# Kernel tuning notes

Measured on AMD Instinct MI355X. Metric: run time of the kernel, lower is better.

Reference implementation:

```python
import jax, jax.numpy as jnp
import numpy as np

WINDOW_SIZE = 5
SIGMA = 1.5


def gaussian_kernel_3d(size, sigma):
    # Faithful replication of the torch code (including its permute quirk):
    # kernel[i,j,k] = exp(-((k-off)^2 + (k-off)^2 + (i-off)^2) / (2*sigma^2))
    c = jnp.arange(size, dtype=jnp.float32) - size // 2
    ci = c[:, None, None]  # axis 0 term (from permute(2,0,1))
    ck = c[None, None, :]  # axis 2 term (coords and permute(1,0,2) coincide)
    g = jnp.exp(-(ck ** 2 + ck ** 2 + ci ** 2) / (2.0 * sigma ** 2))
    g = jnp.broadcast_to(g, (size, size, size))
    return g / g.sum()


def _conv3d(x, w, pad):
    # x: [N,C,D,H,W], w: [O,I,kd,kh,kw]
    return jax.lax.conv_general_dilated(
        x, w, window_strides=(1, 1, 1),
        padding=[(pad, pad)] * 3,
        dimension_numbers=('NCDHW', 'OIDHW', 'NCDHW'))


def setup_inputs() -> dict:
    key = jax.random.key(0)
    k1, k2 = jax.random.split(key)
    img1 = jax.random.uniform(k1, (4, 2, 128, 128, 128), dtype=jnp.float32)
    img2 = jax.random.uniform(k2, (4, 1, 128, 128, 128), dtype=jnp.float32)
    window = gaussian_kernel_3d(WINDOW_SIZE, SIGMA)[None, None]  # [1,1,5,5,5]
    return {"img1": img1, "img2": img2, "window": window}


def reference(img1, img2, window):
    ws = window.shape[-1]
    pad = ws // 2
    x1 = img1[:, 1:2]  # select channel 1, keep dim -> [B,1,D,H,W]
    x2 = img2
    mu1 = _conv3d(x1, window, pad)
    mu2 = _conv3d(x2, window, pad)
    mu1_sq = mu1 * mu1
    mu2_sq = mu2 * mu2
    mu1_mu2 = mu1 * mu2
    sigma1_sq = _conv3d(x1 * x1, window, pad) - mu1_sq
    sigma2_sq = _conv3d(x2 * x2, window, pad) - mu2_sq
    sigma12 = _conv3d(x1 * x2, window, pad) - mu1_mu2
    C1 = 0.01 ** 2
    C2 = 0.03 ** 2
    ssim_map = ((2.0 * mu1_mu2 + C1) * (2.0 * sigma12 + C2)) / (
        (mu1_sq + mu2_sq + C1) * (sigma1_sq + sigma2_sq + C2))
    return 1.0 - jnp.mean(ssim_map)
```

## Files before the change

### kernel.cpp

```cpp
#include <hip/hip_runtime.h>


#define NDIM 128
#define TH 4
#define WR (TH + 4)
#define DSUB 16
#define NHT (NDIM / TH)
#define NDT (NDIM / DSUB)
#define NB 4
#define NBLK (NHT * NDT * NB)

__global__ void factorize_window(const float* __restrict__ w, float* __restrict__ ws) {
    if (threadIdx.x == 0) {
        float w000 = w[0];
        #pragma unroll
        for (int i = 0; i < 5; ++i) ws[i]      = w[i * 25];
        #pragma unroll
        for (int j = 0; j < 5; ++j) ws[5 + j]  = w[j * 5] / w000;
        #pragma unroll
        for (int k = 0; k < 5; ++k) ws[10 + k] = w[k] / w000;
    }
}

__launch_bounds__(256, 4)
__global__ void ssim_main(const float* __restrict__ img1,
                          const float* __restrict__ img2,
                          const float* __restrict__ wfac,
                          float* __restrict__ partials) {
    const int bid = blockIdx.x;
    const int th = bid % NHT;
    const int td = (bid / NHT) % NDT;
    const int b  = bid / (NHT * NDT);

    const int h0 = th * TH, d0 = td * DSUB;
    const float* __restrict__ x1 = img1 + (size_t)(b * 2 + 1) * NDIM * NDIM * NDIM;
    const float* __restrict__ x2 = img2 + (size_t)b * NDIM * NDIM * NDIM;

    float uW[5], vW[5], tW[5];
    #pragma unroll
    for (int i = 0; i < 5; ++i) { uW[i] = wfac[i]; vW[i] = wfac[5 + i]; tW[i] = wfac[10 + i]; }

    __shared__ float sWc[5][WR][NDIM];
    __shared__ float sRed[4];

    const int tid  = threadIdx.x;
    const int wrow = tid >> 5;
    const int wcg  = tid & 31;
    const int c0   = wcg * 4;
    const int ghw  = h0 + wrow - 2;
    const int orow = tid >> 6;
    const int oc   = (tid & 63) * 2;

    float2 ring[5][5];
    float2 accS = make_float2(0.f, 0.f);

#define PHASE(I, P) do {                                                       \
    const int i_ = (I);                                                        \
    const int d_ = d0 - 2 + i_;                                                \
    float4 A0 = make_float4(0,0,0,0), A1 = A0, A2 = A0;                        \
    float4 B0 = A0, B1 = A0, B2 = A0;                                          \
    if (((unsigned)d_ < NDIM) && ((unsigned)ghw < NDIM)) {                     \
        const float* __restrict__ r1_ = x1 + ((size_t)d_ * NDIM + ghw) * NDIM; \
        const float* __restrict__ r2_ = x2 + ((size_t)d_ * NDIM + ghw) * NDIM; \
        if (wcg > 0)  { A0 = *(const float4*)(r1_ + c0 - 4);                   \
                        B0 = *(const float4*)(r2_ + c0 - 4); }                 \
        A1 = *(const float4*)(r1_ + c0);                                       \
        B1 = *(const float4*)(r2_ + c0);                                       \
        if (wcg < 31) { A2 = *(const float4*)(r1_ + c0 + 4);                   \
                        B2 = *(const float4*)(r2_ + c0 + 4); }                 \
    }                                                                          \
    float ra[12] = {A0.x,A0.y,A0.z,A0.w, A1.x,A1.y,A1.z,A1.w,                  \
                    A2.x,A2.y,A2.z,A2.w};                                      \
    float rb[12] = {B0.x,B0.y,B0.z,B0.w, B1.x,B1.y,B1.z,B1.w,                  \
                    B2.x,B2.y,B2.z,B2.w};                                      \
    float m1v[4], m2v[4], q11v[4], q22v[4], q12v[4];                           \
    _Pragma("unroll")                                                          \
    for (int k_ = 0; k_ < 4; ++k_) {                                           \
        float m1_=0.f, m2_=0.f, q11_=0.f, q22_=0.f, q12_=0.f;                  \
        _Pragma("unroll")                                                      \
        for (int c_ = 0; c_ < 5; ++c_) {                                       \
            const float a_ = ra[k_ + c_ + 2], b_ = rb[k_ + c_ + 2];            \
            const float ta_ = tW[c_] * a_, tb_ = tW[c_] * b_;                  \
            m1_ += ta_; m2_ += tb_;                                            \
            q11_ += ta_ * a_; q22_ += tb_ * b_; q12_ += ta_ * b_;              \
        }                                                                      \
        m1v[k_]=m1_; m2v[k_]=m2_; q11v[k_]=q11_; q22v[k_]=q22_; q12v[k_]=q12_; \
    }                                                                          \
    __syncthreads();                   \
    *(float4*)&sWc[0][wrow][c0] = make_float4(m1v[0],m1v[1],m1v[2],m1v[3]);    \
    *(float4*)&sWc[1][wrow][c0] = make_float4(m2v[0],m2v[1],m2v[2],m2v[3]);    \
    *(float4*)&sWc[2][wrow][c0] = make_float4(q11v[0],q11v[1],q11v[2],q11v[3]);\
    *(float4*)&sWc[3][wrow][c0] = make_float4(q22v[0],q22v[1],q22v[2],q22v[3]);\
    *(float4*)&sWc[4][wrow][c0] = make_float4(q12v[0],q12v[1],q12v[2],q12v[3]);\
    __syncthreads();                                       \
    _Pragma("unroll")                                                          \
    for (int f_ = 0; f_ < 5; ++f_) {                                           \
        float2 F_ = make_float2(0.f, 0.f);                                     \
        _Pragma("unroll")                                                      \
        for (int r_ = 0; r_ < 5; ++r_) {                                       \
            const float2 wv_ = *(const float2*)&sWc[f_][orow + r_][oc];        \
            F_.x += vW[r_] * wv_.x;                                            \
            F_.y += vW[r_] * wv_.y;                                            \
        }                                                                      \
        ring[(P)][f_] = F_;                                                    \
    }                                                                          \
    if (i_ >= 4) {                                                             \
        float2 F0 = make_float2(0,0), F1 = F0, F2 = F0, F3 = F0, F4 = F0;      \
        _Pragma("unroll")                                                      \
        for (int j_ = 0; j_ < 5; ++j_) {                                       \
            const int s_ = ((P) + 1 + j_) % 5;                                 \
            const float uw_ = uW[j_];                                          \
            F0.x += uw_*ring[s_][0].x; F0.y += uw_*ring[s_][0].y;              \
            F1.x += uw_*ring[s_][1].x; F1.y += uw_*ring[s_][1].y;              \
            F2.x += uw_*ring[s_][2].x; F2.y += uw_*ring[s_][2].y;              \
            F3.x += uw_*ring[s_][3].x; F3.y += uw_*ring[s_][3].y;              \
            F4.x += uw_*ring[s_][4].x; F4.y += uw_*ring[s_][4].y;              \
        }                                                                      \
        {                                                                      \
            const float mu1 = F0.x, mu2 = F1.x;                                \
            const float m11 = mu1*mu1, m22 = mu2*mu2, m12 = mu1*mu2;           \
            const float num = (2.f*m12 + 1e-4f) * (2.f*(F4.x - m12) + 9e-4f);  \
            const float den = (m11 + m22 + 1e-4f) *                            \
                              ((F2.x - m11) + (F3.x - m22) + 9e-4f);           \
            accS.x += __fdividef(num, den);                                    \
        }                                                                      \
        {                                                                      \
            const float mu1 = F0.y, mu2 = F1.y;                                \
            const float m11 = mu1*mu1, m22 = mu2*mu2, m12 = mu1*mu2;           \
            const float num = (2.f*m12 + 1e-4f) * (2.f*(F4.y - m12) + 9e-4f);  \
            const float den = (m11 + m22 + 1e-4f) *                            \
                              ((F2.y - m11) + (F3.y - m22) + 9e-4f);           \
            accS.y += __fdividef(num, den);                                    \
        }                                                                      \
    }                                                                          \
} while (0)

    for (int io = 0; io < 4; ++io) {
        const int ib = io * 5;
        PHASE(ib + 0, 0);
        PHASE(ib + 1, 1);
        PHASE(ib + 2, 2);
        PHASE(ib + 3, 3);
        PHASE(ib + 4, 4);
    }
#undef PHASE

    float acc = accS.x + accS.y;
    #pragma unroll
    for (int off = 32; off > 0; off >>= 1)
        acc += __shfl_down(acc, off, 64);
    __syncthreads();
    if ((tid & 63) == 0) sRed[tid >> 6] = acc;
    __syncthreads();
    if (tid == 0) partials[bid] = sRed[0] + sRed[1] + sRed[2] + sRed[3];
}

__global__ void finalize_kernel(const float* __restrict__ partials, float* __restrict__ out) {
    const int tid = threadIdx.x;
    double s = 0.0;
    for (int i = tid; i < NBLK; i += 256) s += (double)partials[i];
    #pragma unroll
    for (int off = 32; off > 0; off >>= 1)
        s += __shfl_down(s, off, 64);
    __shared__ double sm[4];
    if ((tid & 63) == 0) sm[tid >> 6] = s;
    __syncthreads();
    if (tid == 0)
        out[0] = 1.0f - (float)((sm[0] + sm[1] + sm[2] + sm[3]) / (double)(4LL * 128 * 128 * 128));
}

extern "C" void kernel_launch(void* const* d_in, const int* in_sizes, int n_in,
                              void* d_out, int out_size, void* d_ws, size_t ws_size,
                              hipStream_t stream) {
    const float* img1 = (const float*)d_in[0];
    const float* img2 = (const float*)d_in[1];
    const float* win  = (const float*)d_in[2];
    float* out = (float*)d_out;
    float* ws  = (float*)d_ws;
    float* wfac     = ws;
    float* partials = ws + 16;

    hipLaunchKernelGGL(factorize_window, dim3(1), dim3(64), 0, stream, win, wfac);
    hipLaunchKernelGGL(ssim_main, dim3(NBLK), dim3(256), 0, stream, img1, img2, wfac, partials);
    hipLaunchKernelGGL(finalize_kernel, dim3(1), dim3(256), 0, stream, partials, out);
}
```

Baseline: 162.6 us.

## Double-buffer shared tile, prefetch next depth slice, fuse final reduction via atomics

Each depth slice's global loads are now issued into registers one phase ahead, so they overlap with the current slice's shared-memory stores and vertical pass. The shared staging buffer is double-buffered, which removes one of the two barriers per phase. The separate finalize kernel is replaced by a double atomicAdd plus a last-block counter, which saves a launch. In exchange, shared memory per block doubles, which may lower occupancy, and the prefetch registers add register pressure.

```diff
diff --git a/kernel.cpp b/kernel.cpp
--- a/kernel.cpp
+++ b/kernel.cpp
@@ -10,23 +10,25 @@
 #define NB 4
 #define NBLK (NHT * NDT * NB)
 
-__global__ void factorize_window(const float* __restrict__ w, float* __restrict__ ws) {
+__global__ void setup_kernel(const float* __restrict__ w, float* __restrict__ ws) {
     if (threadIdx.x == 0) {
-        float w000 = w[0];
+        const float w000 = w[0];
         #pragma unroll
         for (int i = 0; i < 5; ++i) ws[i]      = w[i * 25];
         #pragma unroll
         for (int j = 0; j < 5; ++j) ws[5 + j]  = w[j * 5] / w000;
         #pragma unroll
         for (int k = 0; k < 5; ++k) ws[10 + k] = w[k] / w000;
+        *(double*)(ws + 16)       = 0.0;
+        *(unsigned int*)(ws + 18) = 0u;
     }
 }
 
 __launch_bounds__(256, 4)
 __global__ void ssim_main(const float* __restrict__ img1,
                           const float* __restrict__ img2,
-                          const float* __restrict__ wfac,
-                          float* __restrict__ partials) {
+                          float* __restrict__ wsp,
+                          float* __restrict__ out) {
     const int bid = blockIdx.x;
     const int th = bid % NHT;
     const int td = (bid / NHT) % NDT;
@@ -38,10 +40,9 @@
 
     float uW[5], vW[5], tW[5];
     #pragma unroll
-    for (int i = 0; i < 5; ++i) { uW[i] = wfac[i]; vW[i] = wfac[5 + i]; tW[i] = wfac[10 + i]; }
+    for (int i = 0; i < 5; ++i) { uW[i] = wsp[i]; vW[i] = wsp[5 + i]; tW[i] = wsp[10 + i]; }
 
-    __shared__ float sWc[5][WR][NDIM];
-    __shared__ float sRed[4];
+    __shared__ float sWc[2][5][WR][NDIM];
 
     const int tid  = threadIdx.x;
     const int wrow = tid >> 5;
@@ -53,26 +54,33 @@
 
     float2 ring[5][5];
     float2 accS = make_float2(0.f, 0.f);
+    float4 ld[6];
 
-#define PHASE(I, P) do {                                                       \
+#define LOADP(IN) do {                                                         \
+    const int ip_ = (IN);                                                      \
+    const int dp_ = d0 - 2 + ip_;                                              \
+    const float4 z_ = make_float4(0.f, 0.f, 0.f, 0.f);                         \
+    ld[0]=z_; ld[1]=z_; ld[2]=z_; ld[3]=z_; ld[4]=z_; ld[5]=z_;                \
+    if ((ip_ < DSUB + 4) && ((unsigned)dp_ < NDIM) && ((unsigned)ghw < NDIM)) {\
+        const float* __restrict__ r1_ = x1 + ((size_t)dp_ * NDIM + ghw) * NDIM;\
+        const float* __restrict__ r2_ = x2 + ((size_t)dp_ * NDIM + ghw) * NDIM;\
+        if (wcg > 0)  { ld[0] = *(const float4*)(r1_ + c0 - 4);                \
+                        ld[3] = *(const float4*)(r2_ + c0 - 4); }              \
+        ld[1] = *(const float4*)(r1_ + c0);                                    \
+        ld[4] = *(const float4*)(r2_ + c0);                                    \
+        if (wcg < 31) { ld[2] = *(const float4*)(r1_ + c0 + 4);                \
+                        ld[5] = *(const float4*)(r2_ + c0 + 4); }              \
+    }                                                                          \
+} while (0)
+
+#define PHASE(I, P, B) do {                                                    \
     const int i_ = (I);                                                        \
-    const int d_ = d0 - 2 + i_;                                                \
-    float4 A0 = make_float4(0,0,0,0), A1 = A0, A2 = A0;                        \
-    float4 B0 = A0, B1 = A0, B2 = A0;                                          \
-    if (((unsigned)d_ < NDIM) && ((unsigned)ghw < NDIM)) {                     \
-        const float* __restrict__ r1_ = x1 + ((size_t)d_ * NDIM + ghw) * NDIM; \
-        const float* __restrict__ r2_ = x2 + ((size_t)d_ * NDIM + ghw) * NDIM; \
-        if (wcg > 0)  { A0 = *(const float4*)(r1_ + c0 - 4);                   \
-                        B0 = *(const float4*)(r2_ + c0 - 4); }                 \
-        A1 = *(const float4*)(r1_ + c0);                                       \
-        B1 = *(const float4*)(r2_ + c0);                                       \
-        if (wcg < 31) { A2 = *(const float4*)(r1_ + c0 + 4);                   \
-                        B2 = *(const float4*)(r2_ + c0 + 4); }                 \
-    }                                                                          \
-    float ra[12] = {A0.x,A0.y,A0.z,A0.w, A1.x,A1.y,A1.z,A1.w,                  \
-                    A2.x,A2.y,A2.z,A2.w};                                      \
-    float rb[12] = {B0.x,B0.y,B0.z,B0.w, B1.x,B1.y,B1.z,B1.w,                  \
-                    B2.x,B2.y,B2.z,B2.w};                                      \
+    float ra[12] = {ld[0].x,ld[0].y,ld[0].z,ld[0].w,                           \
+                    ld[1].x,ld[1].y,ld[1].z,ld[1].w,                           \
+                    ld[2].x,ld[2].y,ld[2].z,ld[2].w};                          \
+    float rb[12] = {ld[3].x,ld[3].y,ld[3].z,ld[3].w,                           \
+                    ld[4].x,ld[4].y,ld[4].z,ld[4].w,                           \
+                    ld[5].x,ld[5].y,ld[5].z,ld[5].w};                          \
     float m1v[4], m2v[4], q11v[4], q22v[4], q12v[4];                           \
     _Pragma("unroll")                                                          \
     for (int k_ = 0; k_ < 4; ++k_) {                                           \
@@ -86,23 +94,23 @@
         }                                                                      \
         m1v[k_]=m1_; m2v[k_]=m2_; q11v[k_]=q11_; q22v[k_]=q22_; q12v[k_]=q12_; \
     }                                                                          \
-    __syncthreads();                   \
-    *(float4*)&sWc[0][wrow][c0] = make_float4(m1v[0],m1v[1],m1v[2],m1v[3]);    \
-    *(float4*)&sWc[1][wrow][c0] = make_float4(m2v[0],m2v[1],m2v[2],m2v[3]);    \
-    *(float4*)&sWc[2][wrow][c0] = make_float4(q11v[0],q11v[1],q11v[2],q11v[3]);\
-    *(float4*)&sWc[3][wrow][c0] = make_float4(q22v[0],q22v[1],q22v[2],q22v[3]);\
-    *(float4*)&sWc[4][wrow][c0] = make_float4(q12v[0],q12v[1],q12v[2],q12v[3]);\
-    __syncthreads();                                       \
+    LOADP(i_ + 1);    \
+    *(float4*)&sWc[B][0][wrow][c0] = make_float4(m1v[0],m1v[1],m1v[2],m1v[3]); \
+    *(float4*)&sWc[B][1][wrow][c0] = make_float4(m2v[0],m2v[1],m2v[2],m2v[3]); \
+    *(float4*)&sWc[B][2][wrow][c0] = make_float4(q11v[0],q11v[1],q11v[2],q11v[3]);\
+    *(float4*)&sWc[B][3][wrow][c0] = make_float4(q22v[0],q22v[1],q22v[2],q22v[3]);\
+    *(float4*)&sWc[B][4][wrow][c0] = make_float4(q12v[0],q12v[1],q12v[2],q12v[3]);\
+    __syncthreads();            \
     _Pragma("unroll")                                                          \
     for (int f_ = 0; f_ < 5; ++f_) {                                           \
         float2 F_ = make_float2(0.f, 0.f);                                     \
         _Pragma("unroll")                                                      \
         for (int r_ = 0; r_ < 5; ++r_) {                                       \
-            const float2 wv_ = *(const float2*)&sWc[f_][orow + r_][oc];        \
+            const float2 wv_ = *(const float2*)&sWc[B][f_][orow + r_][oc];     \
             F_.x += vW[r_] * wv_.x;                                            \
             F_.y += vW[r_] * wv_.y;                                            \
         }                                                                      \
-        ring[(P)][f_] = F_;                                                    \
+        ring[P][f_] = F_;                                                      \
     }                                                                          \
     if (i_ >= 4) {                                                             \
         float2 F0 = make_float2(0,0), F1 = F0, F2 = F0, F3 = F0, F4 = F0;      \
@@ -135,38 +143,43 @@
     }                                                                          \
 } while (0)
 
-    for (int io = 0; io < 4; ++io) {
-        const int ib = io * 5;
-        PHASE(ib + 0, 0);
-        PHASE(ib + 1, 1);
-        PHASE(ib + 2, 2);
-        PHASE(ib + 3, 3);
-        PHASE(ib + 4, 4);
+    LOADP(0);
+    for (int io = 0; io < 2; ++io) {
+        const int ib = io * 10;
+        PHASE(ib + 0, 0, 0);
+        PHASE(ib + 1, 1, 1);
+        PHASE(ib + 2, 2, 0);
+        PHASE(ib + 3, 3, 1);
+        PHASE(ib + 4, 4, 0);
+        PHASE(ib + 5, 0, 1);
+        PHASE(ib + 6, 1, 0);
+        PHASE(ib + 7, 2, 1);
+        PHASE(ib + 8, 3, 0);
+        PHASE(ib + 9, 4, 1);
     }
 #undef PHASE
+#undef LOADP
 
     float acc = accS.x + accS.y;
     #pragma unroll
     for (int off = 32; off > 0; off >>= 1)
         acc += __shfl_down(acc, off, 64);
     __syncthreads();
-    if ((tid & 63) == 0) sRed[tid >> 6] = acc;
+    float* sred = &sWc[0][0][0][0];
+    if ((tid & 63) == 0) sred[tid >> 6] = acc;
     __syncthreads();
-    if (tid == 0) partials[bid] = sRed[0] + sRed[1] + sRed[2] + sRed[3];
-}
-
-__global__ void finalize_kernel(const float* __restrict__ partials, float* __restrict__ out) {
-    const int tid = threadIdx.x;
-    double s = 0.0;
-    for (int i = tid; i < NBLK; i += 256) s += (double)partials[i];
-    #pragma unroll
-    for (int off = 32; off > 0; off >>= 1)
-        s += __shfl_down(s, off, 64);
-    __shared__ double sm[4];
-    if ((tid & 63) == 0) sm[tid >> 6] = s;
-    __syncthreads();
-    if (tid == 0)
-        out[0] = 1.0f - (float)((sm[0] + sm[1] + sm[2] + sm[3]) / (double)(4LL * 128 * 128 * 128));
+    if (tid == 0) {
+        const float bsum = sred[0] + sred[1] + sred[2] + sred[3];
+        double* accg      = (double*)(wsp + 16);
+        unsigned int* cnt = (unsigned int*)(wsp + 18);
+        atomicAdd(accg, (double)bsum);
+        __threadfence();
+        const unsigned int prev = atomicAdd(cnt, 1u);
+        if (prev == (unsigned int)(NBLK - 1)) {
+            const double total = atomicAdd(accg, 0.0);
+            out[0] = 1.0f - (float)(total / (double)(4LL * NDIM * NDIM * NDIM));
+        }
+    }
 }
 
 extern "C" void kernel_launch(void* const* d_in, const int* in_sizes, int n_in,
@@ -177,10 +190,8 @@
     const float* win  = (const float*)d_in[2];
     float* out = (float*)d_out;
     float* ws  = (float*)d_ws;
-    float* wfac     = ws;
-    float* partials = ws + 16;
 
-    hipLaunchKernelGGL(factorize_window, dim3(1), dim3(64), 0, stream, win, wfac);
-    hipLaunchKernelGGL(ssim_main, dim3(NBLK), dim3(256), 0, stream, img1, img2, wfac, partials);
-    hipLaunchKernelGGL(finalize_kernel, dim3(1), dim3(256), 0, stream, partials, out);
+    hipLaunchKernelGGL(setup_kernel, dim3(1), dim3(64), 0, stream, win, ws);
+    hipLaunchKernelGGL(ssim_main, dim3(NBLK), dim3(256), 0, stream,
+                       img1, img2, ws, out);
 }
```

New measurement: 444.9 us. 2.74x slower.
